# Kernel tuning notes

Measured on AMD Instinct MI355X. Metric: run time of the kernel, lower is better.

The kernel has to match this reference:

```python
import jax, jax.numpy as jnp
import numpy as np

N_HEADS = 16
WINDOW = 256
GLOBAL_IDX = np.array([0])

def _global_local_mask(seq_len):
    # allowed[i,j] = True if |i-j|<=window OR i is global OR j is global
    i = jnp.arange(seq_len)[:, None]
    j = jnp.arange(seq_len)[None, :]
    g = jnp.asarray(GLOBAL_IDX)
    row_global = jnp.isin(jnp.arange(seq_len), g)
    allowed = (jnp.abs(i - j) <= WINDOW) | row_global[:, None] | row_global[None, :]
    return allowed

def setup_inputs() -> dict:
    key = jax.random.key(0)
    ks = jax.random.split(key, 9)
    B, S, D = 1, 2048, 1024
    w = 0.02
    return {
        "x": jax.random.normal(ks[0], (B, S, D), jnp.float32),
        "Wq": jax.random.normal(ks[1], (D, D), jnp.float32) * w,
        "bq": jnp.zeros((D,), jnp.float32),
        "Wk": jax.random.normal(ks[2], (D, D), jnp.float32) * w,
        "bk": jnp.zeros((D,), jnp.float32),
        "Wv": jax.random.normal(ks[3], (D, D), jnp.float32) * w,
        "bv": jnp.zeros((D,), jnp.float32),
        "Wo": jax.random.normal(ks[4], (D, D), jnp.float32) * w,
        "bo": jnp.zeros((D,), jnp.float32),
    }

def reference(x, Wq, bq, Wk, bk, Wv, bv, Wo, bo):
    B, S, D = x.shape
    H = N_HEADS
    Dh = D // H
    scale = Dh ** -0.5
    # projections (torch Linear: y = x @ W^T + b; here W stored as [in,out] equivalent)
    q = (x @ Wq + bq).reshape(B, S, H, Dh)
    k = (x @ Wk + bk).reshape(B, S, H, Dh)
    v = (x @ Wv + bv).reshape(B, S, H, Dh)
    # dense scores [B,H,S,S]
    scores = jnp.einsum("bqhd,bkhd->bhqk", q, k) * scale
    allowed = _global_local_mask(S)  # [S,S] bool
    scores = jnp.where(allowed[None, None], scores, -jnp.inf)
    attn = jax.nn.softmax(scores, axis=-1)
    out = jnp.einsum("bhqk,bkhd->bqhd", attn, v).reshape(B, S, D)
    return out @ Wo + bo
```

## Files before the change

### kernel.cpp

```cpp
#include <hip/hip_runtime.h>
#include <hip/hip_bf16.h>
#include <math.h>

#define S_LEN   2048
#define DM      1024
#define NH      16
#define DH      64
#define WIN     256

typedef __attribute__((ext_vector_type(8))) short          bf16x8;
typedef __attribute__((ext_vector_type(4))) float          f32x4;
typedef __attribute__((ext_vector_type(8))) unsigned short u16x8;
typedef __attribute__((ext_vector_type(4))) unsigned short u16x4;
typedef unsigned short u16;

#define GLDS(gsrc, ldst)                                                        \
    __builtin_amdgcn_global_load_lds(                                           \
        (const __attribute__((address_space(1))) void*)(gsrc),                  \
        (__attribute__((address_space(3))) void*)(ldst), 16, 0, 0)

__device__ __forceinline__ u16 f2bf(float f) {
    union { float f; unsigned u; } v; v.f = f;
    unsigned r = v.u + 0x7FFF + ((v.u >> 16) & 1);
    return (u16)(r >> 16);
}

__global__ __launch_bounds__(256) void cvt_x_kernel(const float* __restrict__ x,
                                                    u16* __restrict__ xb) {
    int i = (blockIdx.x * 256 + threadIdx.x) * 8;
    float4 a = *(const float4*)&x[i];
    float4 b = *(const float4*)&x[i + 4];
    u16x8 o;
    o[0] = f2bf(a.x); o[1] = f2bf(a.y); o[2] = f2bf(a.z); o[3] = f2bf(a.w);
    o[4] = f2bf(b.x); o[5] = f2bf(b.y); o[6] = f2bf(b.z); o[7] = f2bf(b.w);
    *(u16x8*)&xb[i] = o;
}

__global__ __launch_bounds__(256) void cvt_wT_kernel(const float* __restrict__ Wq,
                                                     const float* __restrict__ Wk,
                                                     const float* __restrict__ Wv,
                                                     const float* __restrict__ Wo,
                                                     u16* __restrict__ WT) {
    __shared__ float Ws[64][65];
    const float* W = (blockIdx.z == 0) ? Wq : (blockIdx.z == 1) ? Wk
                   : (blockIdx.z == 2) ? Wv : Wo;
    u16* dst = WT + (size_t)blockIdx.z * (1u << 20);
    const int k0 = blockIdx.x * 64, n0 = blockIdx.y * 64;
    const int tid = threadIdx.x;
#pragma unroll
    for (int p = 0; p < 4; ++p) {
        int flat = tid + p * 256;
        int row = flat >> 4, c4 = (flat & 15) * 4;
        float4 v = *(const float4*)&W[(k0 + row) * DM + n0 + c4];
        Ws[row][c4 + 0] = v.x; Ws[row][c4 + 1] = v.y;
        Ws[row][c4 + 2] = v.z; Ws[row][c4 + 3] = v.w;
    }
    __syncthreads();
#pragma unroll
    for (int p = 0; p < 4; ++p) {
        int flat = tid + p * 256;
        int n = flat >> 4, k4 = (flat & 15) * 4;
        u16x4 o;
#pragma unroll
        for (int j = 0; j < 4; ++j) o[j] = f2bf(Ws[k4 + j][n]);
        *(u16x4*)&dst[(n0 + n) * DM + k0 + k4] = o;
    }
}

template<int OMODE>
__device__ __forceinline__ void gemm_mfma_body(const u16* __restrict__ A,
                                               const u16* __restrict__ Bt,
                                               const float* __restrict__ bias,
                                               u16* __restrict__ Cb,
                                               float* __restrict__ Cf) {
    __shared__ __align__(16) u16 As[64 * 64];
    __shared__ __align__(16) u16 Bs[128 * 64];
    const int tid = threadIdx.x;
    const int l = tid & 63, w = tid >> 6;
    const int wm = w >> 1, wn = w & 1;
    const int l15 = l & 15, lh = l >> 4;
    const int brow = blockIdx.y * 64, bcol = blockIdx.x * 128;

    f32x4 acc[2][4];
#pragma unroll
    for (int i = 0; i < 2; ++i)
#pragma unroll
        for (int j = 0; j < 4; ++j) acc[i][j] = (f32x4)0.f;

    const int lr = l >> 3, lc = l & 7, g = lc ^ lr;
    const u16* aSrc = A  + (size_t)(brow + w * 16 + lr) * DM + g * 8;
    const u16* bSrc = Bt + (size_t)(bcol + w * 32 + lr) * DM + g * 8;

    for (int k0 = 0; k0 < DM; k0 += 64) {
        __syncthreads();
#pragma unroll
        for (int i = 0; i < 2; ++i)
            GLDS(aSrc + i * 8 * DM + k0, &As[(w * 2 + i) * 512]);
#pragma unroll
        for (int i = 0; i < 4; ++i)
            GLDS(bSrc + i * 8 * DM + k0, &Bs[(w * 4 + i) * 512]);
        __syncthreads();

#pragma unroll
        for (int ks = 0; ks < 2; ++ks) {
            bf16x8 af[2], bf[4];
#pragma unroll
            for (int i = 0; i < 2; ++i) {
                int ra = wm * 32 + i * 16 + l15;
                af[i] = *(const bf16x8*)&As[ra * 64 + (((ks * 4 + lh) ^ (ra & 7)) * 8)];
            }
#pragma unroll
            for (int j = 0; j < 4; ++j) {
                int rb = wn * 64 + j * 16 + l15;
                bf[j] = *(const bf16x8*)&Bs[rb * 64 + (((ks * 4 + lh) ^ (rb & 7)) * 8)];
            }
#pragma unroll
            for (int i = 0; i < 2; ++i)
#pragma unroll
                for (int j = 0; j < 4; ++j)
                    acc[i][j] = __builtin_amdgcn_mfma_f32_16x16x32_bf16(af[i], bf[j], acc[i][j], 0, 0, 0);
        }
    }
#pragma unroll
    for (int j = 0; j < 4; ++j) {
        int gcol = bcol + wn * 64 + j * 16 + l15;
        float bz = bias[gcol];
#pragma unroll
        for (int i = 0; i < 2; ++i) {
            int grow = brow + wm * 32 + i * 16 + lh * 4;
            if (OMODE == 2) {
                u16x4 tv;
#pragma unroll
                for (int rr = 0; rr < 4; ++rr) tv[rr] = f2bf(acc[i][j][rr] + bz);
                *(u16x4*)&Cb[(size_t)gcol * S_LEN + grow] = tv;
            } else {
#pragma unroll
                for (int rr = 0; rr < 4; ++rr) {
                    float v = acc[i][j][rr] + bz;
                    if (OMODE == 0) Cb[(grow + rr) * DM + gcol] = f2bf(v);
                    else            Cf[(grow + rr) * DM + gcol] = v;
                }
            }
        }
    }
}

__global__ __launch_bounds__(256) void qkv_mfma_kernel(
        const u16* __restrict__ xb,
        const u16* __restrict__ WqT, const float* __restrict__ bq, u16* __restrict__ Qb,
        const u16* __restrict__ WkT, const float* __restrict__ bk, u16* __restrict__ Kb,
        const u16* __restrict__ WvT, const float* __restrict__ bv, u16* __restrict__ VT) {
    if (blockIdx.z == 0)      gemm_mfma_body<0>(xb, WqT, bq, Qb, nullptr);
    else if (blockIdx.z == 1) gemm_mfma_body<0>(xb, WkT, bk, Kb, nullptr);
    else                      gemm_mfma_body<2>(xb, WvT, bv, VT, nullptr);
}

__global__ __launch_bounds__(256) void oproj_mfma_kernel(
        const u16* __restrict__ Ob, const u16* __restrict__ WoT,
        const float* __restrict__ bo, float* __restrict__ out) {
    gemm_mfma_body<1>(Ob, WoT, bo, nullptr, out);
}

__global__ __launch_bounds__(256) void attn_mfma_kernel(
        const u16* __restrict__ Qb, const u16* __restrict__ Kb,
        const u16* __restrict__ VT, u16* __restrict__ Ob) {
    __shared__ __align__(16) u16 Ks[2][64 * 64];
    __shared__ __align__(16) u16 Vs[2][64 * 64];
    __shared__ __align__(16) u16 Pl[4 * 16 * 72];
    const int tid = threadIdx.x;
    const int w = tid >> 6, l = tid & 63;
    const int l15 = l & 15, lh = l >> 4;

    const int swz = (blockIdx.x & 7) * 64 + (blockIdx.x >> 3);
    const int h = swz >> 5, i0 = (swz & 31) * 64;
    const int q0 = i0 + w * 16;
    u16* Pw = &Pl[w * 16 * 72];

    bf16x8 qf[2];
    {
        int qr = q0 + l15;
        qf[0] = *(const bf16x8*)&Qb[qr * DM + h * DH + lh * 8];
        qf[1] = *(const bf16x8*)&Qb[qr * DM + h * DH + 32 + lh * 8];
    }

    f32x4 o[4];
    float ls[4] = {0.f, 0.f, 0.f, 0.f};
#pragma unroll
    for (int fc = 0; fc < 4; ++fc) o[fc] = (f32x4)0.f;

    int t_lo, t_hi;
    {
        int lo = i0 - WIN;      if (lo < 0) lo = 0;
        int hi = i0 + 63 + WIN; if (hi > S_LEN - 1) hi = S_LEN - 1;
        if (i0 == 0) hi = S_LEN - 1;
        t_lo = lo >> 6; t_hi = hi >> 6;
    }
    const int nband = t_hi - t_lo + 1;
    const int nt = nband + (t_lo > 0 ? 1 : 0);
    int wt_hi;
    {
        int whi = q0 + 15 + WIN; if (whi > S_LEN - 1) whi = S_LEN - 1;
        wt_hi = whi >> 6;
    }
    const bool isglob = (q0 == 0);

    const int lr = l >> 3, g = (l & 7) ^ lr;

    int cur = 0;
    {
        const int j0 = t_lo << 6;
#pragma unroll
        for (int c2 = 0; c2 < 2; ++c2) {
            int c = w * 2 + c2;
            GLDS(&Kb[(size_t)(j0 + c * 8 + lr) * DM + h * DH + g * 8], &Ks[0][c * 512]);
            GLDS(&VT[(size_t)(h * DH + c * 8 + lr) * S_LEN + j0 + g * 8], &Vs[0][c * 512]);
        }
    }
    __syncthreads();

    for (int it = 0; it < nt; ++it) {
        const int t = (it < nband) ? (t_lo + it) : 0;
        const int j0 = t << 6;

        if (it + 1 < nt) {
            const int jn = ((it + 1 < nband) ? (t_lo + it + 1) : 0) << 6;
            u16* KsB = Ks[cur ^ 1];
            u16* VsB = Vs[cur ^ 1];
#pragma unroll
            for (int c2 = 0; c2 < 2; ++c2) {
                int c = w * 2 + c2;
                GLDS(&Kb[(size_t)(jn + c * 8 + lr) * DM + h * DH + g * 8], &KsB[c * 512]);
                GLDS(&VT[(size_t)(h * DH + c * 8 + lr) * S_LEN + jn + g * 8], &VsB[c * 512]);
            }
        }

        if (isglob || it >= nband || t <= wt_hi) {
            const u16* Kc = Ks[cur];
            const u16* Vc = Vs[cur];

            f32x4 s[4];
#pragma unroll
            for (int fc = 0; fc < 4; ++fc) s[fc] = (f32x4)0.f;
#pragma unroll
            for (int ks = 0; ks < 2; ++ks)
#pragma unroll
                for (int fc = 0; fc < 4; ++fc) {
                    int rb = fc * 16 + l15;
                    bf16x8 kf = *(const bf16x8*)&Kc[rb * 64 + (((ks * 4 + lh) ^ (rb & 7)) * 8)];
                    s[fc] = __builtin_amdgcn_mfma_f32_16x16x32_bf16(qf[ks], kf, s[fc], 0, 0, 0);
                }

#pragma unroll
            for (int fc = 0; fc < 4; ++fc)
#pragma unroll
                for (int rr = 0; rr < 4; ++rr) {
                    int r = q0 + lh * 4 + rr;
                    int c = j0 + fc * 16 + l15;
                    int d = r - c;
                    bool ok = (d <= WIN && -d <= WIN) || (r == 0) || (c == 0);
                    s[fc][rr] = ok ? __expf(s[fc][rr] * 0.125f) : 0.f;
                }
#pragma unroll
            for (int rr = 0; rr < 4; ++rr)
                ls[rr] += (s[0][rr] + s[1][rr]) + (s[2][rr] + s[3][rr]);

#pragma unroll
            for (int fc = 0; fc < 4; ++fc)
#pragma unroll
                for (int rr = 0; rr < 4; ++rr)
                    Pw[(lh * 4 + rr) * 72 + fc * 16 + l15] = f2bf(s[fc][rr]);
            asm volatile("s_waitcnt lgkmcnt(0)" ::: "memory");

#pragma unroll
            for (int ks = 0; ks < 2; ++ks) {
                bf16x8 pa = *(const bf16x8*)&Pw[l15 * 72 + ks * 32 + lh * 8];
#pragma unroll
                for (int fc = 0; fc < 4; ++fc) {
                    int rb = fc * 16 + l15;
                    bf16x8 vfr = *(const bf16x8*)&Vc[rb * 64 + (((ks * 4 + lh) ^ (rb & 7)) * 8)];
                    o[fc] = __builtin_amdgcn_mfma_f32_16x16x32_bf16(pa, vfr, o[fc], 0, 0, 0);
                }
            }
        }

        __syncthreads();
        cur ^= 1;
    }

#pragma unroll
    for (int rr = 0; rr < 4; ++rr)
#pragma unroll
        for (int mk = 1; mk < 16; mk <<= 1)
            ls[rr] += __shfl_xor(ls[rr], mk, 64);

#pragma unroll
    for (int rr = 0; rr < 4; ++rr) {
        float inv = 1.0f / ls[rr];
#pragma unroll
        for (int fc = 0; fc < 4; ++fc)
            Ob[(q0 + lh * 4 + rr) * DM + h * DH + fc * 16 + l15] = f2bf(o[fc][rr] * inv);
    }
}

extern "C" void kernel_launch(void* const* d_in, const int* in_sizes, int n_in,
                              void* d_out, int out_size, void* d_ws, size_t ws_size,
                              hipStream_t stream) {
    const float* x  = (const float*)d_in[0];
    const float* Wq = (const float*)d_in[1];
    const float* bq = (const float*)d_in[2];
    const float* Wk = (const float*)d_in[3];
    const float* bk = (const float*)d_in[4];
    const float* Wv = (const float*)d_in[5];
    const float* bv = (const float*)d_in[6];
    const float* Wo = (const float*)d_in[7];
    const float* bo = (const float*)d_in[8];
    float* out = (float*)d_out;

    char* W = (char*)d_ws;
    u16* xb  = (u16*)(W);
    u16* WT  = (u16*)(W + ((size_t)4  << 20));
    u16* Qb  = (u16*)(W + ((size_t)12 << 20));
    u16* Kb  = (u16*)(W + ((size_t)16 << 20));
    u16* VT  = (u16*)(W + ((size_t)20 << 20));
    u16* Ob  = xb;
    const u16* WqT = WT;
    const u16* WkT = WT + (1u << 20);
    const u16* WvT = WT + (2u << 20);
    const u16* WoT = WT + (3u << 20);

    cvt_x_kernel <<<dim3(S_LEN * DM / (256 * 8)), 256, 0, stream>>>(x, xb);
    cvt_wT_kernel<<<dim3(16, 16, 4), 256, 0, stream>>>(Wq, Wk, Wv, Wo, WT);
    qkv_mfma_kernel<<<dim3(8, 32, 3), 256, 0, stream>>>(xb, WqT, bq, Qb,
                                                        WkT, bk, Kb, WvT, bv, VT);
    attn_mfma_kernel<<<dim3(512), 256, 0, stream>>>(Qb, Kb, VT, Ob);
    oproj_mfma_kernel<<<dim3(8, 32), 256, 0, stream>>>(Ob, WoT, bo, out);
}
```

Before: 168.8 us.

## Double-buffer GEMM LDS tiles and split global-row attention across idle warps

The projection GEMM now double-buffers its A/B shared-memory tiles, so the next k-slice is prefetched while MFMAs run on the current one, leaving one barrier per iteration. In attention, the first query block no longer scans all 32 key tiles serially. Its band runs as usual, and warps 1-3 compute the global row 0 over the remaining tiles in scalar code, then merge partial sums through shared memory. This is meant to remove the long tail from the single block that covered the whole sequence, at the cost of extra LDS and a scalar path that skips max subtraction.

```diff
diff --git a/kernel.cpp b/kernel.cpp
--- a/kernel.cpp
+++ b/kernel.cpp
@@ -23,6 +23,9 @@
     union { float f; unsigned u; } v; v.f = f;
     unsigned r = v.u + 0x7FFF + ((v.u >> 16) & 1);
     return (u16)(r >> 16);
+}
+__device__ __forceinline__ float bf2f(u16 x) {
+    union { unsigned u; float f; } v; v.u = ((unsigned)x) << 16; return v.f;
 }
 
 __global__ __launch_bounds__(256) void cvt_x_kernel(const float* __restrict__ x,
@@ -73,8 +76,8 @@
                                                const float* __restrict__ bias,
                                                u16* __restrict__ Cb,
                                                float* __restrict__ Cf) {
-    __shared__ __align__(16) u16 As[64 * 64];
-    __shared__ __align__(16) u16 Bs[128 * 64];
+    __shared__ __align__(16) u16 As[2][64 * 64];
+    __shared__ __align__(16) u16 Bs[2][128 * 64];
     const int tid = threadIdx.x;
     const int l = tid & 63, w = tid >> 6;
     const int wm = w >> 1, wn = w & 1;
@@ -91,15 +94,23 @@
     const u16* aSrc = A  + (size_t)(brow + w * 16 + lr) * DM + g * 8;
     const u16* bSrc = Bt + (size_t)(bcol + w * 32 + lr) * DM + g * 8;
 
-    for (int k0 = 0; k0 < DM; k0 += 64) {
-        __syncthreads();
-#pragma unroll
-        for (int i = 0; i < 2; ++i)
-            GLDS(aSrc + i * 8 * DM + k0, &As[(w * 2 + i) * 512]);
-#pragma unroll
-        for (int i = 0; i < 4; ++i)
-            GLDS(bSrc + i * 8 * DM + k0, &Bs[(w * 4 + i) * 512]);
-        __syncthreads();
+#pragma unroll
+    for (int i = 0; i < 2; ++i) GLDS(aSrc + i * 8 * DM, &As[0][(w * 2 + i) * 512]);
+#pragma unroll
+    for (int i = 0; i < 4; ++i) GLDS(bSrc + i * 8 * DM, &Bs[0][(w * 4 + i) * 512]);
+    __syncthreads();
+
+    int cur = 0;
+    for (int kt = 0; kt < 16; ++kt) {
+        if (kt + 1 < 16) {
+            const int kn = (kt + 1) * 64;
+#pragma unroll
+            for (int i = 0; i < 2; ++i)
+                GLDS(aSrc + i * 8 * DM + kn, &As[cur ^ 1][(w * 2 + i) * 512]);
+#pragma unroll
+            for (int i = 0; i < 4; ++i)
+                GLDS(bSrc + i * 8 * DM + kn, &Bs[cur ^ 1][(w * 4 + i) * 512]);
+        }
 
 #pragma unroll
         for (int ks = 0; ks < 2; ++ks) {
@@ -107,12 +118,12 @@
 #pragma unroll
             for (int i = 0; i < 2; ++i) {
                 int ra = wm * 32 + i * 16 + l15;
-                af[i] = *(const bf16x8*)&As[ra * 64 + (((ks * 4 + lh) ^ (ra & 7)) * 8)];
+                af[i] = *(const bf16x8*)&As[cur][ra * 64 + (((ks * 4 + lh) ^ (ra & 7)) * 8)];
             }
 #pragma unroll
             for (int j = 0; j < 4; ++j) {
                 int rb = wn * 64 + j * 16 + l15;
-                bf[j] = *(const bf16x8*)&Bs[rb * 64 + (((ks * 4 + lh) ^ (rb & 7)) * 8)];
+                bf[j] = *(const bf16x8*)&Bs[cur][rb * 64 + (((ks * 4 + lh) ^ (rb & 7)) * 8)];
             }
 #pragma unroll
             for (int i = 0; i < 2; ++i)
@@ -120,7 +131,10 @@
                 for (int j = 0; j < 4; ++j)
                     acc[i][j] = __builtin_amdgcn_mfma_f32_16x16x32_bf16(af[i], bf[j], acc[i][j], 0, 0, 0);
         }
-    }
+        __syncthreads();
+        cur ^= 1;
+    }
+
 #pragma unroll
     for (int j = 0; j < 4; ++j) {
         int gcol = bcol + wn * 64 + j * 16 + l15;
@@ -167,6 +181,8 @@
     __shared__ __align__(16) u16 Ks[2][64 * 64];
     __shared__ __align__(16) u16 Vs[2][64 * 64];
     __shared__ __align__(16) u16 Pl[4 * 16 * 72];
+    __shared__ float MBo[3][64];
+    __shared__ float MBl[3];
     const int tid = threadIdx.x;
     const int w = tid >> 6, l = tid & 63;
     const int l15 = l & 15, lh = l >> 4;
@@ -175,6 +191,7 @@
     const int h = swz >> 5, i0 = (swz & 31) * 64;
     const int q0 = i0 + w * 16;
     u16* Pw = &Pl[w * 16 * 72];
+    const bool g0 = (i0 == 0);
 
     bf16x8 qf[2];
     {
@@ -192,17 +209,10 @@
     {
         int lo = i0 - WIN;      if (lo < 0) lo = 0;
         int hi = i0 + 63 + WIN; if (hi > S_LEN - 1) hi = S_LEN - 1;
-        if (i0 == 0) hi = S_LEN - 1;
         t_lo = lo >> 6; t_hi = hi >> 6;
     }
     const int nband = t_hi - t_lo + 1;
     const int nt = nband + (t_lo > 0 ? 1 : 0);
-    int wt_hi;
-    {
-        int whi = q0 + 15 + WIN; if (whi > S_LEN - 1) whi = S_LEN - 1;
-        wt_hi = whi >> 6;
-    }
-    const bool isglob = (q0 == 0);
 
     const int lr = l >> 3, g = (l & 7) ^ lr;
 
@@ -234,7 +244,7 @@
             }
         }
 
-        if (isglob || it >= nband || t <= wt_hi) {
+        {
             const u16* Kc = Ks[cur];
             const u16* Vc = Vs[cur];
 
@@ -287,11 +297,69 @@
         cur ^= 1;
     }
 
+    if (g0 && w > 0) {
+        bf16x8 q0p[8];
+#pragma unroll
+        for (int c = 0; c < 8; ++c)
+            q0p[c] = *(const bf16x8*)&Qb[h * DH + c * 8];
+        float op = 0.f, lp = 0.f;
+        float* sb = (float*)Pw;
+        for (int t = 5 + (w - 1); t < 32; t += 3) {
+            const int j0 = t * 64;
+            float sacc = 0.f;
+            const u16* krow = &Kb[(size_t)(j0 + l) * DM + h * DH];
+#pragma unroll
+            for (int c = 0; c < 8; ++c) {
+                bf16x8 kc = *(const bf16x8*)&krow[c * 8];
+#pragma unroll
+                for (int e = 0; e < 8; ++e)
+                    sacc = fmaf(bf2f((u16)q0p[c][e]), bf2f((u16)kc[e]), sacc);
+            }
+            float sv = __expf(sacc * 0.125f);
+            lp += sv;
+            sb[l] = sv;
+            asm volatile("s_waitcnt lgkmcnt(0)" ::: "memory");
+            const u16* vrow = &VT[(size_t)(h * DH + l) * S_LEN + j0];
+#pragma unroll
+            for (int c = 0; c < 8; ++c) {
+                bf16x8 vc = *(const bf16x8*)&vrow[c * 8];
+                f32x4 sA = *(const f32x4*)&sb[c * 8];
+                f32x4 sB = *(const f32x4*)&sb[c * 8 + 4];
+                op = fmaf(sA[0], bf2f((u16)vc[0]), op);
+                op = fmaf(sA[1], bf2f((u16)vc[1]), op);
+                op = fmaf(sA[2], bf2f((u16)vc[2]), op);
+                op = fmaf(sA[3], bf2f((u16)vc[3]), op);
+                op = fmaf(sB[0], bf2f((u16)vc[4]), op);
+                op = fmaf(sB[1], bf2f((u16)vc[5]), op);
+                op = fmaf(sB[2], bf2f((u16)vc[6]), op);
+                op = fmaf(sB[3], bf2f((u16)vc[7]), op);
+            }
+            asm volatile("s_waitcnt lgkmcnt(0)" ::: "memory");
+        }
+#pragma unroll
+        for (int mk = 1; mk < 64; mk <<= 1) lp += __shfl_xor(lp, mk, 64);
+        MBo[w - 1][l] = op;
+        if (l == 0) MBl[w - 1] = lp;
+    }
+    __syncthreads();
+
+    float G = 0.f;
+    if (g0 && w == 0) {
+        G = MBl[0] + MBl[1] + MBl[2];
+        if (lh == 0) {
+#pragma unroll
+            for (int fc = 0; fc < 4; ++fc)
+                o[fc][0] += MBo[0][fc * 16 + l15] + MBo[1][fc * 16 + l15]
+                          + MBo[2][fc * 16 + l15];
+        }
+    }
+
 #pragma unroll
     for (int rr = 0; rr < 4; ++rr)
 #pragma unroll
         for (int mk = 1; mk < 16; mk <<= 1)
             ls[rr] += __shfl_xor(ls[rr], mk, 64);
+    if (g0 && w == 0 && lh == 0) ls[0] += G;
 
 #pragma unroll
     for (int rr = 0; rr < 4; ++rr) {
```

Result: slower. 203.6 us (+20.6%).
